# Kernel tuning notes

Hardware: AMD Instinct MI355X
Metric: run time of the kernel (lower is better)

Reference implementation:

```python
import jax, jax.numpy as jnp
import numpy as np

D_MODEL = 1024
N_HEADS = 16
D_HEAD = D_MODEL // N_HEADS
B, S = 4, 2048


def setup_inputs() -> dict:
    key = jax.random.key(0)
    ks = jax.random.split(key, 9)
    s = 1.0 / np.sqrt(D_MODEL)
    inp = {
        "x": jax.random.normal(ks[0], (B, S, D_MODEL), dtype=jnp.float32),
        "W_q": jax.random.uniform(ks[1], (D_MODEL, D_MODEL), jnp.float32, -s, s),
        "b_q": jax.random.uniform(ks[2], (D_MODEL,), jnp.float32, -s, s),
        "W_k": jax.random.uniform(ks[3], (D_MODEL, D_MODEL), jnp.float32, -s, s),
        "b_k": jax.random.uniform(ks[4], (D_MODEL,), jnp.float32, -s, s),
        "W_v": jax.random.uniform(ks[5], (D_MODEL, D_MODEL), jnp.float32, -s, s),
        "b_v": jax.random.uniform(ks[6], (D_MODEL,), jnp.float32, -s, s),
        "W_o": jax.random.uniform(ks[7], (D_MODEL, D_MODEL), jnp.float32, -s, s),
        "b_o": jax.random.uniform(ks[8], (D_MODEL,), jnp.float32, -s, s),
    }
    return inp


def reference(x, W_q, b_q, W_k, b_k, W_v, b_v, W_o, b_o):
    b, s, d = x.shape
    # Project and split heads: [b, h, s, d_head]
    def split(t):
        return t.reshape(b, s, N_HEADS, D_HEAD).transpose(0, 2, 1, 3)
    Q = split(x @ W_q + b_q)
    K = split(x @ W_k + b_k)
    V = split(x @ W_v + b_v)
    scores = jnp.einsum('bhqd,bhkd->bhqk', Q, K) / np.sqrt(D_HEAD).astype(np.float32)
    causal = jnp.triu(jnp.full((s, s), -jnp.inf, dtype=scores.dtype), k=1)
    scores = scores + causal
    attn = jax.nn.softmax(scores, axis=-1)  # dropout p=0 -> identity
    ctx = jnp.einsum('bhqk,bhkd->bhqd', attn, V)
    ctx = ctx.transpose(0, 2, 1, 3).reshape(b, s, d)
    return ctx @ W_o + b_o
```

## Files before the change

kernel.cpp:

```cpp
#include <hip/hip_runtime.h>
#include <stdint.h>

#define B_    4
#define S_    2048
#define DM    1024
#define NH    16
#define DH    64
#define BH    (B_ * NH)
#define MROWS (B_ * S_)
#define LOG2E 1.4426950408889634f

typedef __attribute__((ext_vector_type(8))) short short8;
typedef __attribute__((ext_vector_type(4))) float f32x4;
typedef __attribute__((ext_vector_type(16))) float f32x16;
typedef __attribute__((ext_vector_type(4))) unsigned int u32x4;

__device__ __forceinline__ unsigned short f2bf(float f) {
  unsigned int u = __float_as_uint(f);
  u = (u + 0x7FFFu + ((u >> 16) & 1u)) >> 16;
  return (unsigned short)u;
}
__device__ __forceinline__ unsigned int pack_bf16(float lo, float hi) {
  unsigned int a = (__float_as_uint(lo) + 0x8000u) >> 16;
  unsigned int b = (__float_as_uint(hi) + 0x8000u) & 0xFFFF0000u;
  return a | b;
}

__device__ __forceinline__ void gll16(const void* g, const void* l) {
  __builtin_amdgcn_global_load_lds(
      (__attribute__((address_space(1))) void*)(unsigned long long)g,
      (__attribute__((address_space(3))) void*)(unsigned int)(unsigned long long)l,
      16, 0, 0);
}

__global__ __launch_bounds__(256) void prep_kernel(
    const float* __restrict__ x,
    const float* __restrict__ Wq, const float* __restrict__ Wk,
    const float* __restrict__ Wv, const float* __restrict__ Wo,
    unsigned short* __restrict__ xb,
    unsigned short* __restrict__ wt_qkv, unsigned short* __restrict__ wt_o) {
  __shared__ float t[32][33];
  const int z = blockIdx.z;
  if (z >= 4) {
    size_t lb = (size_t)(z - 4) * 1024 + blockIdx.y * 32 + blockIdx.x;
    size_t i = (lb * 256 + threadIdx.x) * 8;
    float4 a = *(const float4*)(x + i);
    float4 b = *(const float4*)(x + i + 4);
    short8 o;
    o[0] = (short)f2bf(a.x); o[1] = (short)f2bf(a.y);
    o[2] = (short)f2bf(a.z); o[3] = (short)f2bf(a.w);
    o[4] = (short)f2bf(b.x); o[5] = (short)f2bf(b.y);
    o[6] = (short)f2bf(b.z); o[7] = (short)f2bf(b.w);
    *(short8*)(xb + i) = o;
    return;
  }
  const float* W = z == 0 ? Wq : z == 1 ? Wk : z == 2 ? Wv : Wo;
  unsigned short* dst = z < 3 ? wt_qkv + (size_t)z * DM * DM : wt_o;
  const int nb = blockIdx.x * 32, kb = blockIdx.y * 32;
  const int tx = threadIdx.x & 31, ty = threadIdx.x >> 5;
#pragma unroll
  for (int p = 0; p < 4; ++p) {
    int r = ty + p * 8;
    t[r][tx] = W[(size_t)(kb + r) * DM + nb + tx];
  }
  __syncthreads();
#pragma unroll
  for (int p = 0; p < 4; ++p) {
    int r = ty + p * 8;
    dst[(size_t)(nb + r) * DM + kb + tx] = f2bf(t[tx][r]);
  }
}

__device__ __forceinline__ void gemm_core(const unsigned short* __restrict__ A,
                                          const unsigned short* __restrict__ Bt,
                                          int m0, int n0,
                                          unsigned short* As, unsigned short* Bs,
                                          f32x16 (&acc)[2][2]) {
  const int tid = threadIdx.x;
  const int lane = tid & 63, wave = tid >> 6;
  const int l31 = lane & 31, half = lane >> 5;
  const int wm = (wave >> 1) * 64, wn = (wave & 1) * 64;

  for (int kk = 0; kk < DM; kk += 64) {
#pragma unroll
    for (int p = 0; p < 4; ++p) {
      int idx = p * 256 + tid;
      int row = idx >> 3, ch = idx & 7;
      int sc = (ch ^ (row & 7)) << 3;
      gll16(A  + (size_t)(m0 + row) * DM + kk + sc, As + idx * 8);
      gll16(Bt + (size_t)(n0 + row) * DM + kk + sc, Bs + idx * 8);
    }
    __syncthreads();
#pragma unroll
    for (int ks = 0; ks < 4; ++ks) {
      short8 af[2], bf[2];
#pragma unroll
      for (int mi = 0; mi < 2; ++mi) {
        int row = wm + mi * 32 + l31;
        af[mi] = *(const short8*)&As[row * 64 + (((ks * 2 + half) ^ (l31 & 7)) << 3)];
      }
#pragma unroll
      for (int nj = 0; nj < 2; ++nj) {
        int row = wn + nj * 32 + l31;
        bf[nj] = *(const short8*)&Bs[row * 64 + (((ks * 2 + half) ^ (l31 & 7)) << 3)];
      }
#pragma unroll
      for (int mi = 0; mi < 2; ++mi)
#pragma unroll
        for (int nj = 0; nj < 2; ++nj)
          acc[mi][nj] = __builtin_amdgcn_mfma_f32_32x32x16_bf16(af[mi], bf[nj], acc[mi][nj], 0, 0, 0);
    }
    __syncthreads();
  }
}

__global__ __launch_bounds__(256) void gemm_qkv_kernel(
    const unsigned short* __restrict__ xb, const unsigned short* __restrict__ wt,
    const float* __restrict__ bq, const float* __restrict__ bk, const float* __restrict__ bv,
    unsigned short* __restrict__ Qb, unsigned short* __restrict__ Kb,
    unsigned short* __restrict__ Vt) {
  __shared__ unsigned short As[128 * 64];
  __shared__ unsigned short Bs[128 * 64];
  f32x16 acc[2][2] = {};
  const int m0 = blockIdx.y * 128, n0 = blockIdx.x * 128;
  gemm_core(xb, wt, m0, n0, As, Bs, acc);

  const int tid = threadIdx.x, lane = tid & 63, wave = tid >> 6;
  const int l31 = lane & 31, half = lane >> 5;
  const int wm = (wave >> 1) * 64, wn = (wave & 1) * 64;
  const int which = n0 >> 10;
  const int nb = n0 - (which << 10);
  if (which == 2) {
#pragma unroll
    for (int nj = 0; nj < 2; ++nj) {
      int n10 = nb + wn + nj * 32 + l31;
      float bsv = bv[n10];
      int h = n10 >> 6, d = n10 & 63;
#pragma unroll
      for (int mi = 0; mi < 2; ++mi) {
#pragma unroll
        for (int reg = 0; reg < 16; ++reg) {
          int m = m0 + wm + mi * 32 + (reg & 3) + 8 * (reg >> 2) + 4 * half;
          int b = m >> 11, s = m & 2047;
          Vt[(((size_t)(b * NH + h)) * DH + d) * S_ + s] = f2bf(acc[mi][nj][reg] + bsv);
        }
      }
    }
    return;
  }
  const float* bias = which == 0 ? bq : bk;
  unsigned short* dst = which == 0 ? Qb : Kb;
  const float scale = (which == 0) ? 0.125f * LOG2E : 1.0f;
#pragma unroll
  for (int nj = 0; nj < 2; ++nj) {
    int n10 = nb + wn + nj * 32 + l31;
    float bsv = bias[n10];
    int h = n10 >> 6, d = n10 & 63;
#pragma unroll
    for (int mi = 0; mi < 2; ++mi) {
#pragma unroll
      for (int reg = 0; reg < 16; ++reg) {
        int m = m0 + wm + mi * 32 + (reg & 3) + 8 * (reg >> 2) + 4 * half;
        int b = m >> 11, s = m & 2047;
        float v = (acc[mi][nj][reg] + bsv) * scale;
        dst[(((size_t)(b * NH + h)) * S_ + s) * DH + d] = f2bf(v);
      }
    }
  }
}

__global__ __launch_bounds__(256) void gemm_out_kernel(
    const unsigned short* __restrict__ ctx, const unsigned short* __restrict__ wto,
    const float* __restrict__ bo, float* __restrict__ out) {
  __shared__ unsigned short As[128 * 64];
  __shared__ unsigned short Bs[128 * 64];
  f32x16 acc[2][2] = {};
  const int m0 = blockIdx.y * 128, n0 = blockIdx.x * 128;
  gemm_core(ctx, wto, m0, n0, As, Bs, acc);

  const int tid = threadIdx.x, lane = tid & 63, wave = tid >> 6;
  const int l31 = lane & 31, half = lane >> 5;
  const int wm = (wave >> 1) * 64, wn = (wave & 1) * 64;
#pragma unroll
  for (int nj = 0; nj < 2; ++nj) {
    int n = n0 + wn + nj * 32 + l31;
    float bsv = bo[n];
#pragma unroll
    for (int mi = 0; mi < 2; ++mi) {
#pragma unroll
      for (int reg = 0; reg < 16; ++reg) {
        int m = m0 + wm + mi * 32 + (reg & 3) + 8 * (reg >> 2) + 4 * half;
        out[(size_t)m * DM + n] = acc[mi][nj][reg] + bsv;
      }
    }
  }
}


#define TTILE(T, PAE, PAO) do {                                              \
    f32x16 sa;                                                               \
    _Pragma("unroll") for (int r = 0; r < 16; ++r) sa[r] = -8.f;             \
    {                                                                        \
      int row = (T) * 32 + l31;                                              \
      _Pragma("unroll") for (int ks = 0; ks < 4; ++ks) {                     \
        short8 kf = *(const short8*)&Ks[row * 64 +                           \
                      (((ks * 2 + half) ^ (row & 7)) << 3)];                 \
        sa = __builtin_amdgcn_mfma_f32_32x32x16_bf16(kf, qf[ks], sa, 0, 0, 0);\
      }                                                                      \
    }                                                                        \
    if (kt == qt) {                                                          \
      int ql = wave * 32 + l31;                                              \
      _Pragma("unroll") for (int r = 0; r < 16; ++r) {                       \
        int kv = (T) * 32 + (r & 3) + 8 * (r >> 2) + 4 * half;               \
        if (kv > ql) sa[r] = -__builtin_inff();                              \
      }                                                                      \
    }                                                                        \
    float p[16];                                                             \
    _Pragma("unroll") for (int r = 0; r < 16; ++r)                           \
      p[r] = __builtin_amdgcn_exp2f(sa[r]);                                  \
    la0 += p[0] + p[4] + p[8]  + p[12];                                      \
    la1 += p[1] + p[5] + p[9]  + p[13];                                      \
    la2 += p[2] + p[6] + p[10] + p[14];                                      \
    la3 += p[3] + p[7] + p[11] + p[15];                                      \
    {                                                                        \
      unsigned int A0 = pack_bf16(p[0], p[1]), A1 = pack_bf16(p[2], p[3]);   \
      unsigned int B0 = pack_bf16(p[4], p[5]), B1 = pack_bf16(p[6], p[7]);   \
      unsigned int A0x = (unsigned int)__shfl_xor((int)A0, 32);              \
      unsigned int A1x = (unsigned int)__shfl_xor((int)A1, 32);              \
      unsigned int B0x = (unsigned int)__shfl_xor((int)B0, 32);              \
      unsigned int B1x = (unsigned int)__shfl_xor((int)B1, 32);              \
      u32x4 fa;                                                              \
      fa[0] = half ? B0x : A0;                                               \
      fa[1] = half ? B1x : A1;                                               \
      fa[2] = half ? B0  : A0x;                                              \
      fa[3] = half ? B1  : A1x;                                              \
      PAE = __builtin_bit_cast(short8, fa);                                  \
    }                                                                        \
    {                                                                        \
      unsigned int C0 = pack_bf16(p[8], p[9]),   C1 = pack_bf16(p[10], p[11]);\
      unsigned int D0 = pack_bf16(p[12], p[13]), D1 = pack_bf16(p[14], p[15]);\
      unsigned int C0x = (unsigned int)__shfl_xor((int)C0, 32);              \
      unsigned int C1x = (unsigned int)__shfl_xor((int)C1, 32);              \
      unsigned int D0x = (unsigned int)__shfl_xor((int)D0, 32);              \
      unsigned int D1x = (unsigned int)__shfl_xor((int)D1, 32);              \
      u32x4 fb;                                                              \
      fb[0] = half ? D0x : C0;                                               \
      fb[1] = half ? D1x : C1;                                               \
      fb[2] = half ? D0  : C0x;                                              \
      fb[3] = half ? D1  : C1x;                                              \
      PAO = __builtin_bit_cast(short8, fb);                                  \
    }                                                                        \
  } while (0)

#define PVSTEP(S2, PA) do {                                                  \
    int c = (S2) * 2 + half;                                                 \
    {                                                                        \
      int row = l31;                                                         \
      short8 vf = *(const short8*)&Vs[row * 128 +                            \
                    (((c & 8) | ((c ^ row) & 7)) << 3)];                     \
      o0 = __builtin_amdgcn_mfma_f32_32x32x16_bf16(PA, vf, o0, 0, 0, 0);     \
    }                                                                        \
    {                                                                        \
      int row = 32 + l31;                                                    \
      short8 vf = *(const short8*)&Vs[row * 128 +                            \
                    (((c & 8) | ((c ^ row) & 7)) << 3)];                     \
      o1 = __builtin_amdgcn_mfma_f32_32x32x16_bf16(PA, vf, o1, 0, 0, 0);     \
    }                                                                        \
  } while (0)

__global__ __launch_bounds__(256, 2) void attn_kernel(
    const unsigned short* __restrict__ Qb, const unsigned short* __restrict__ Kb,
    const unsigned short* __restrict__ Vt, unsigned short* __restrict__ ctx) {
  __shared__ unsigned short Ks[128 * 64];
  __shared__ unsigned short Vs[64 * 128];

  const int tid = threadIdx.x, lane = tid & 63, wave = tid >> 6;
  const int l31 = lane & 31, half = lane >> 5;
  const int bh = blockIdx.x;
  const int qt = 15 - blockIdx.y;
  const int b = bh >> 4, h = bh & 15;

  const unsigned short* Qp = Qb + ((size_t)bh * S_ + qt * 128) * DH;
  const unsigned short* Kbase = Kb + (size_t)bh * S_ * DH;
  const unsigned short* Vbase = Vt + (size_t)bh * DH * S_;

#pragma unroll
  for (int p = 0; p < 4; ++p) {
    int idx = p * 256 + tid;
    int row = idx >> 3, ch = idx & 7;
    int sc = (ch ^ (row & 7)) << 3;
    gll16(Kbase + row * 64 + sc, Ks + idx * 8);
  }
  short8 qf[4];
#pragma unroll
  for (int ks = 0; ks < 4; ++ks)
    qf[ks] = *(const short8*)(Qp + (wave * 32 + l31) * 64 + ks * 16 + half * 8);
  __syncthreads();

  f32x16 o0 = {}, o1 = {};
  float la0 = 0.f, la1 = 0.f, la2 = 0.f, la3 = 0.f;

  for (int kt = 0; kt <= qt; ++kt) {
    const unsigned short* Vp = Vbase + kt * 128;
#pragma unroll
    for (int p = 0; p < 4; ++p) {
      int idx = p * 256 + tid;
      int row = idx >> 4, ch = idx & 15;
      int sc = (ch & 8) | ((ch ^ row) & 7);
      gll16(Vp + (size_t)row * S_ + sc * 8, Vs + idx * 8);
    }

    short8 pa0, pa1, pa2, pa3, pa4, pa5, pa6, pa7;
    TTILE(0, pa0, pa1);
    TTILE(1, pa2, pa3);
    TTILE(2, pa4, pa5);
    TTILE(3, pa6, pa7);

    __syncthreads();

    if (kt < qt) {
      const unsigned short* Kp = Kbase + (size_t)(kt + 1) * 128 * DH;
#pragma unroll
      for (int p = 0; p < 4; ++p) {
        int idx = p * 256 + tid;
        int row = idx >> 3, ch = idx & 7;
        int sc = (ch ^ (row & 7)) << 3;
        gll16(Kp + row * 64 + sc, Ks + idx * 8);
      }
    }

    PVSTEP(0, pa0); PVSTEP(1, pa1); PVSTEP(2, pa2); PVSTEP(3, pa3);
    PVSTEP(4, pa4); PVSTEP(5, pa5); PVSTEP(6, pa6); PVSTEP(7, pa7);

    __syncthreads();
  }

  float l = (la0 + la1) + (la2 + la3);
  l += __shfl_xor(l, 32);
#pragma unroll
  for (int r = 0; r < 16; ++r) {
    int qrow = (r & 3) + 8 * (r >> 2) + 4 * half;
    float lr = __shfl(l, qrow);
    float inv = __builtin_amdgcn_rcpf(lr);
    int s = qt * 128 + wave * 32 + qrow;
    ctx[((size_t)(b * S_ + s)) * DM + h * DH + l31]      = f2bf(o0[r] * inv);
    ctx[((size_t)(b * S_ + s)) * DM + h * DH + 32 + l31] = f2bf(o1[r] * inv);
  }
}

extern "C" void kernel_launch(void* const* d_in, const int* in_sizes, int n_in,
                              void* d_out, int out_size, void* d_ws, size_t ws_size,
                              hipStream_t stream) {
  (void)in_sizes; (void)n_in; (void)out_size; (void)ws_size;
  const float* x  = (const float*)d_in[0];
  const float* Wq = (const float*)d_in[1];
  const float* bq = (const float*)d_in[2];
  const float* Wk = (const float*)d_in[3];
  const float* bk = (const float*)d_in[4];
  const float* Wv = (const float*)d_in[5];
  const float* bv = (const float*)d_in[6];
  const float* Wo = (const float*)d_in[7];
  const float* bo = (const float*)d_in[8];
  float* out = (float*)d_out;

  char* ws = (char*)d_ws;
  size_t off = 0;
  auto carve = [&](size_t bytes) -> char* {
    char* p = ws + off;
    off += (bytes + 255) & ~(size_t)255;
    return p;
  };
  unsigned short* xb  = (unsigned short*)carve((size_t)MROWS * DM * 2);
  unsigned short* wtq = (unsigned short*)carve((size_t)3 * DM * DM * 2);
  unsigned short* wto = (unsigned short*)carve((size_t)DM * DM * 2);
  unsigned short* Qb  = (unsigned short*)carve((size_t)BH * S_ * DH * 2);
  unsigned short* Kb  = (unsigned short*)carve((size_t)BH * S_ * DH * 2);
  unsigned short* Vt  = (unsigned short*)carve((size_t)BH * S_ * DH * 2);
  unsigned short* ctx = (unsigned short*)carve((size_t)BH * S_ * DH * 2);

  prep_kernel<<<dim3(32, 32, 8), 256, 0, stream>>>(x, Wq, Wk, Wv, Wo, xb, wtq, wto);
  gemm_qkv_kernel<<<dim3(24, 64), 256, 0, stream>>>(xb, wtq, bq, bk, bv, Qb, Kb, Vt);
  attn_kernel<<<dim3(64, 16), 256, 0, stream>>>(Qb, Kb, Vt, ctx);
  gemm_out_kernel<<<dim3(8, 64), 256, 0, stream>>>(ctx, wto, bo, out);
}
```

Before: 249.0 us.

## Use 256x256 tiles with double-buffered pipelined loads in QKV GEMM

Replaces the 128x128, 4-wave QKV projection GEMM with a 256x256 tile computed by 8 waves. Global-to-LDS loads are double-buffered and split into four staged quarters, interleaved with MFMA phases separated by barriers, and MFMA sections are raised to higher wave priority. The goal is more operand reuse per tile and hiding load latency behind compute. In exchange the block uses 128KB of LDS, so only one block fits per CU, and the grid drops to 384 blocks, which can leave an uneven tail wave.

```diff
diff --git a/kernel.cpp b/kernel.cpp
--- a/kernel.cpp
+++ b/kernel.cpp
@@ -114,20 +114,142 @@
   }
 }
 
-__global__ __launch_bounds__(256) void gemm_qkv_kernel(
+__device__ __forceinline__ void stage_half(const unsigned short* __restrict__ G,
+                                           size_t grow0, int kk,
+                                           unsigned short* lds, int tid) {
+#pragma unroll
+  for (int ls = 0; ls < 2; ++ls) {
+    int idx = ls * 512 + tid;
+    int rl = idx >> 3, ch = idx & 7;
+    int sc = (ch ^ (rl & 7)) << 3;
+    gll16(G + (grow0 + rl) * DM + kk + sc, lds + idx * 8);
+  }
+}
+
+#define MFMA_BF16_32(a, b, c) __builtin_amdgcn_mfma_f32_32x32x16_bf16(a, b, c, 0, 0, 0)
+#define SBAR() do { __builtin_amdgcn_s_barrier(); __builtin_amdgcn_sched_barrier(0); } while (0)
+
+__device__ __forceinline__ void gemm256_core(const unsigned short* __restrict__ A,
+                                             const unsigned short* __restrict__ Bt,
+                                             int m0, int n0,
+                                             unsigned short* As, unsigned short* Bs,
+                                             f32x16 (&acc)[4][2]) {
+  const int tid = threadIdx.x;
+  const int lane = tid & 63, wave = tid >> 6;
+  const int l31 = lane & 31, half = lane >> 5;
+  const int wm = (wave >> 2) * 128, wn = (wave & 3) * 64;
+  const int NT = DM / 64;
+
+  stage_half(A,  (size_t)m0,        0, As, tid);
+  stage_half(A,  (size_t)m0 + 128,  0, As + 8192, tid);
+  stage_half(Bt, (size_t)n0,        0, Bs, tid);
+  stage_half(Bt, (size_t)n0 + 128,  0, Bs + 8192, tid);
+
+  int p = 0;
+  for (int t = 0; t < NT; ++t, p ^= 1) {
+    unsigned short* Ap = As + p * 16384;
+    unsigned short* Bp = Bs + p * 16384;
+    unsigned short* An = As + (p ^ 1) * 16384;
+    unsigned short* Bn = Bs + (p ^ 1) * 16384;
+    const int kk1 = (t + 1) * 64;
+    const bool pre = (t + 1 < NT);
+
+    short8 af[2][4], bf[4];
+
+    if (pre) {
+      stage_half(A, (size_t)m0, kk1, An, tid);
+      asm volatile("s_waitcnt vmcnt(2)" ::: "memory");
+    } else {
+      asm volatile("s_waitcnt vmcnt(0)" ::: "memory");
+    }
+    SBAR();
+#pragma unroll
+    for (int mi = 0; mi < 2; ++mi) {
+      int row = wm + mi * 32 + l31;
+#pragma unroll
+      for (int ks = 0; ks < 4; ++ks)
+        af[mi][ks] = *(const short8*)&Ap[row * 64 + (((ks * 2 + half) ^ (l31 & 7)) << 3)];
+    }
+    {
+      int row = wn + l31;
+#pragma unroll
+      for (int ks = 0; ks < 4; ++ks)
+        bf[ks] = *(const short8*)&Bp[row * 64 + (((ks * 2 + half) ^ (l31 & 7)) << 3)];
+    }
+    __builtin_amdgcn_s_setprio(1);
+#pragma unroll
+    for (int ks = 0; ks < 4; ++ks) {
+      acc[0][0] = MFMA_BF16_32(af[0][ks], bf[ks], acc[0][0]);
+      acc[1][0] = MFMA_BF16_32(af[1][ks], bf[ks], acc[1][0]);
+    }
+    __builtin_amdgcn_s_setprio(0);
+    SBAR();
+
+    if (pre) stage_half(A, (size_t)m0 + 128, kk1, An + 8192, tid);
+    {
+      int row = wn + 32 + l31;
+#pragma unroll
+      for (int ks = 0; ks < 4; ++ks)
+        bf[ks] = *(const short8*)&Bp[row * 64 + (((ks * 2 + half) ^ (l31 & 7)) << 3)];
+    }
+    __builtin_amdgcn_s_setprio(1);
+#pragma unroll
+    for (int ks = 0; ks < 4; ++ks) {
+      acc[0][1] = MFMA_BF16_32(af[0][ks], bf[ks], acc[0][1]);
+      acc[1][1] = MFMA_BF16_32(af[1][ks], bf[ks], acc[1][1]);
+    }
+    __builtin_amdgcn_s_setprio(0);
+    SBAR();
+
+    if (pre) stage_half(Bt, (size_t)n0, kk1, Bn, tid);
+#pragma unroll
+    for (int mi = 0; mi < 2; ++mi) {
+      int row = wm + 64 + mi * 32 + l31;
+#pragma unroll
+      for (int ks = 0; ks < 4; ++ks)
+        af[mi][ks] = *(const short8*)&Ap[row * 64 + (((ks * 2 + half) ^ (l31 & 7)) << 3)];
+    }
+    __builtin_amdgcn_s_setprio(1);
+#pragma unroll
+    for (int ks = 0; ks < 4; ++ks) {
+      acc[2][1] = MFMA_BF16_32(af[0][ks], bf[ks], acc[2][1]);
+      acc[3][1] = MFMA_BF16_32(af[1][ks], bf[ks], acc[3][1]);
+    }
+    __builtin_amdgcn_s_setprio(0);
+    SBAR();
+
+    if (pre) stage_half(Bt, (size_t)n0 + 128, kk1, Bn + 8192, tid);
+    {
+      int row = wn + l31;
+#pragma unroll
+      for (int ks = 0; ks < 4; ++ks)
+        bf[ks] = *(const short8*)&Bp[row * 64 + (((ks * 2 + half) ^ (l31 & 7)) << 3)];
+    }
+    __builtin_amdgcn_s_setprio(1);
+#pragma unroll
+    for (int ks = 0; ks < 4; ++ks) {
+      acc[2][0] = MFMA_BF16_32(af[0][ks], bf[ks], acc[2][0]);
+      acc[3][0] = MFMA_BF16_32(af[1][ks], bf[ks], acc[3][0]);
+    }
+    __builtin_amdgcn_s_setprio(0);
+    SBAR();
+  }
+}
+
+__global__ __launch_bounds__(512, 2) void gemm_qkv_kernel(
     const unsigned short* __restrict__ xb, const unsigned short* __restrict__ wt,
     const float* __restrict__ bq, const float* __restrict__ bk, const float* __restrict__ bv,
     unsigned short* __restrict__ Qb, unsigned short* __restrict__ Kb,
     unsigned short* __restrict__ Vt) {
-  __shared__ unsigned short As[128 * 64];
-  __shared__ unsigned short Bs[128 * 64];
-  f32x16 acc[2][2] = {};
-  const int m0 = blockIdx.y * 128, n0 = blockIdx.x * 128;
-  gemm_core(xb, wt, m0, n0, As, Bs, acc);
+  __shared__ unsigned short As[2 * 16384];
+  __shared__ unsigned short Bs[2 * 16384];
+  f32x16 acc[4][2] = {};
+  const int m0 = blockIdx.y * 256, n0 = blockIdx.x * 256;
+  gemm256_core(xb, wt, m0, n0, As, Bs, acc);
 
   const int tid = threadIdx.x, lane = tid & 63, wave = tid >> 6;
   const int l31 = lane & 31, half = lane >> 5;
-  const int wm = (wave >> 1) * 64, wn = (wave & 1) * 64;
+  const int wm = (wave >> 2) * 128, wn = (wave & 3) * 64;
   const int which = n0 >> 10;
   const int nb = n0 - (which << 10);
   if (which == 2) {
@@ -137,7 +259,7 @@
       float bsv = bv[n10];
       int h = n10 >> 6, d = n10 & 63;
 #pragma unroll
-      for (int mi = 0; mi < 2; ++mi) {
+      for (int mi = 0; mi < 4; ++mi) {
 #pragma unroll
         for (int reg = 0; reg < 16; ++reg) {
           int m = m0 + wm + mi * 32 + (reg & 3) + 8 * (reg >> 2) + 4 * half;
@@ -157,7 +279,7 @@
     float bsv = bias[n10];
     int h = n10 >> 6, d = n10 & 63;
 #pragma unroll
-    for (int mi = 0; mi < 2; ++mi) {
+    for (int mi = 0; mi < 4; ++mi) {
 #pragma unroll
       for (int reg = 0; reg < 16; ++reg) {
         int m = m0 + wm + mi * 32 + (reg & 3) + 8 * (reg >> 2) + 4 * half;
@@ -379,7 +501,7 @@
   unsigned short* ctx = (unsigned short*)carve((size_t)BH * S_ * DH * 2);
 
   prep_kernel<<<dim3(32, 32, 8), 256, 0, stream>>>(x, Wq, Wk, Wv, Wo, xb, wtq, wto);
-  gemm_qkv_kernel<<<dim3(24, 64), 256, 0, stream>>>(xb, wtq, bq, bk, bv, Qb, Kb, Vt);
+  gemm_qkv_kernel<<<dim3(12, 32), 512, 0, stream>>>(xb, wtq, bq, bk, bv, Qb, Kb, Vt);
   attn_kernel<<<dim3(64, 16), 256, 0, stream>>>(Qb, Kb, Vt, ctx);
   gemm_out_kernel<<<dim3(8, 64), 256, 0, stream>>>(ctx, wto, bo, out);
 }
```

After: 258.0 us. +3.6%, slower.
